# Kernel optimization log

Hardware: AMD Instinct MI355X
Metric: run time of the kernel (lower is better)

The kernel has to match this reference:

```python
import jax, jax.numpy as jnp
import numpy as np

B, N, E, H, AD, V, STEPS = 32, 256, 4, 512, 256, 10000, 5


def setup_inputs() -> dict:
    key = jax.random.key(0)
    ks = jax.random.split(key, 16)
    s = 0.02  # xavier-ish init scale
    return {
        "annotation": jax.random.randint(ks[0], (B, N), 0, V),
        "A": jax.random.normal(ks[1], (B, N, 2 * N * E), dtype=jnp.float32),
        "emb": jax.random.normal(ks[2], (V, AD), dtype=jnp.float32) * s,
        "W_in": jax.random.normal(ks[3], (E, H, H), dtype=jnp.float32) * s,
        "b_in": jnp.zeros((E, H), jnp.float32),
        "W_out": jax.random.normal(ks[4], (E, H, H), dtype=jnp.float32) * s,
        "b_out": jnp.zeros((E, H), jnp.float32),
        "Wr": jax.random.normal(ks[5], (3 * H, H), dtype=jnp.float32) * s,
        "br": jnp.zeros((H,), jnp.float32),
        "Wz": jax.random.normal(ks[6], (3 * H, H), dtype=jnp.float32) * s,
        "bz": jnp.zeros((H,), jnp.float32),
        "Wh": jax.random.normal(ks[7], (3 * H, H), dtype=jnp.float32) * s,
        "bh": jnp.zeros((H,), jnp.float32),
        "Wo": jax.random.normal(ks[8], (H + AD, H), dtype=jnp.float32) * s,
        "bo": jnp.zeros((H,), jnp.float32),
    }


def reference(annotation, A, emb, W_in, b_in, W_out, b_out,
              Wr, br, Wz, bz, Wh, bh, Wo, bo):
    ann = emb[annotation]                                   # [B, N, AD]
    pad = jnp.zeros((B, N, H - AD), ann.dtype)
    prop = jnp.concatenate([ann, pad], axis=2)              # [B, N, H]
    A_in, A_out = A[:, :, :N * E], A[:, :, N * E:]          # [B, N, N*E] each

    for _ in range(STEPS):
        # fused per-edge-type linears: [B, E, N, H] -> [B, E*N, H]
        ins = (jnp.einsum('bnd,edh->benh', prop, W_in)
               + b_in[None, :, None, :]).reshape(B, E * N, H)
        outs = (jnp.einsum('bnd,edh->benh', prop, W_out)
                + b_out[None, :, None, :]).reshape(B, E * N, H)
        a_in = jnp.matmul(A_in, ins)                        # [B, N, H]
        a_out = jnp.matmul(A_out, outs)                     # [B, N, H]
        a = jnp.concatenate([a_in, a_out, prop], axis=2)    # [B, N, 3H]
        r = jax.nn.sigmoid(a @ Wr + br)
        z = jax.nn.sigmoid(a @ Wz + bz)
        j = jnp.concatenate([a_in, a_out, r * prop], axis=2)
        h_hat = jnp.tanh(j @ Wh + bh)
        prop = (1.0 - z) * prop + z * h_hat

    join = jnp.concatenate([prop, ann], axis=2)             # [B, N, H+AD]
    return jnp.tanh(join @ Wo + bo)                         # [B, N, H]
```

## Files before the change

kernel.cpp:

```cpp
#include <hip/hip_runtime.h>
#include <hip/hip_bf16.h>
#include <cstdint>
#include <cstddef>

typedef unsigned short u16;
typedef _Float16 f16;
typedef f16 f16x8 __attribute__((ext_vector_type(8)));
typedef float f32x4 __attribute__((ext_vector_type(4)));

static __device__ inline u16 f2h(float f) {
    f16 h = (f16)f;
    return *reinterpret_cast<u16*>(&h);
}
static __device__ inline float h2f(u16 u) {
    f16 h = *reinterpret_cast<f16*>(&u);
    return (float)h;
}

#define GLL(g, l) __builtin_amdgcn_global_load_lds(                    \
    (const __attribute__((address_space(1))) void*)(g),                \
    (__attribute__((address_space(3))) void*)(l), 16, 0, 0)

static __device__ inline int xcd_swz(int fid, int nwg) {
    const int q = nwg >> 3;
    return (fid & 7) * q + (fid >> 3);
}

static __device__ inline void stage_tile(const u16* __restrict__ src, int ld,
                                         u16* lds, int wave, int lane) {
    const int r = lane >> 2;
    const int c = (lane & 3) << 3;
    const u16* g0 = src + (size_t)(wave * 32 + r) * ld + c;
    GLL(g0, lds + wave * 1024);
    GLL(g0 + (size_t)16 * ld, lds + wave * 1024 + 512);
}

static __device__ inline void compute32(const u16* lA, const u16* lB,
                                        int wq_r, int wq_c, int lr, int lk,
                                        f32x4 acc[4][4]) {
    f16x8 a[4], b[4];
    #pragma unroll
    for (int i = 0; i < 4; ++i)
        a[i] = *reinterpret_cast<const f16x8*>(&lA[(wq_r + i * 16 + lr) * 32 + lk]);
    #pragma unroll
    for (int j = 0; j < 4; ++j)
        b[j] = *reinterpret_cast<const f16x8*>(&lB[(wq_c + j * 16 + lr) * 32 + lk]);
    #pragma unroll
    for (int i = 0; i < 4; ++i)
        #pragma unroll
        for (int j = 0; j < 4; ++j)
            acc[i][j] = __builtin_amdgcn_mfma_f32_16x16x32_f16(a[i], b[j], acc[i][j], 0, 0, 0);
}

static __device__ inline void gemm128(const u16* __restrict__ a1, int lda1, int ka1,
                                      const u16* __restrict__ a2, int lda2,
                                      const u16* __restrict__ bt, int ldb,
                                      int K, int m0, int n0,
                                      u16* sA, u16* sB, f32x4 acc[4][4])
{
    const int t = threadIdx.x, lane = t & 63, wave = t >> 6;
    const int lr = lane & 15, lk = (lane >> 4) << 3;
    const int wq_r = (wave >> 1) << 6, wq_c = (wave & 1) << 6;
    const int nt = K >> 5;
    stage_tile(a1 + (size_t)m0 * lda1, lda1, sA, wave, lane);
    stage_tile(bt + (size_t)n0 * ldb, ldb, sB, wave, lane);
    __syncthreads();
    int buf = 0;
    for (int ti = 0; ti < nt; ++ti) {
        const int k1 = (ti + 1) << 5;
        if (k1 < K) {
            const u16* s;
            int ld;
            if (k1 < ka1) { s = a1 + (size_t)m0 * lda1 + k1;        ld = lda1; }
            else          { s = a2 + (size_t)m0 * lda2 + (k1 - ka1); ld = lda2; }
            stage_tile(s, ld, sA + (buf ^ 1) * 4096, wave, lane);
            stage_tile(bt + (size_t)n0 * ldb + k1, ldb, sB + (buf ^ 1) * 4096, wave, lane);
        }
        compute32(sA + buf * 4096, sB + buf * 4096, wq_r, wq_c, lr, lk, acc);
        __syncthreads();
        buf ^= 1;
    }
}

#define EPI                                         \
    const int lane = threadIdx.x & 63;              \
    const int wave = threadIdx.x >> 6;              \
    const int wq_r = (wave >> 1) << 6;              \
    const int wq_c = (wave & 1) << 6;               \
    const int lr = lane & 15;                       \
    const int l4 = (lane >> 4) << 2;

#define TDIR (32ull * 512 * 1024)

__global__ __launch_bounds__(256, 4) void k_proj(const u16* __restrict__ P,
                                                 const u16* __restrict__ Wio,
                                                 const float* __restrict__ b_in,
                                                 const float* __restrict__ b_out,
                                                 u16* __restrict__ T)
{
    __shared__ u16 sA[2 * 4096], sB[2 * 4096];
    const int fid = xcd_swz(blockIdx.x, gridDim.x);
    const int n = fid & 31, m = fid >> 5;
    const int m0 = m << 7, n0 = n << 7;
    f32x4 acc[4][4] = {};
    gemm128(P, 512, 512, P, 512, Wio, 512, 512, m0, n0, sA, sB, acc);
    EPI
    #pragma unroll
    for (int i = 0; i < 4; ++i) {
        const int row = m0 + wq_r + i * 16 + l4;
        const int b = row >> 8, mm = row & 255;
        #pragma unroll
        for (int j = 0; j < 4; ++j) {
            const int col = n0 + wq_c + j * 16 + lr;
            const int dir = col >> 11, eh = col & 2047;
            const float bia = (dir ? b_out : b_in)[eh];
            const int e = eh >> 9, h = eh & 511;
            ushort4 w4;
            w4.x = f2h(acc[i][j][0] + bia);
            w4.y = f2h(acc[i][j][1] + bia);
            w4.z = f2h(acc[i][j][2] + bia);
            w4.w = f2h(acc[i][j][3] + bia);
            u16* dst = T + (size_t)dir * TDIR + (size_t)b * 512 * 1024 + (size_t)h * 1024 + e * 256 + mm;
            *reinterpret_cast<ushort4*>(dst) = w4;
        }
    }
}

__global__ __launch_bounds__(256, 4) void k_amat(const u16* __restrict__ A16,
                                                 const u16* __restrict__ T,
                                                 u16* __restrict__ acat)
{
    __shared__ u16 sA[2 * 4096], sB[2 * 4096];
    const int fid = xcd_swz(blockIdx.x, gridDim.x);
    const int n = fid & 3, m = (fid >> 2) & 1, bd = fid >> 3;
    const int b = bd >> 1, dir = bd & 1;
    const int m0 = m << 7, n0 = n << 7;
    const u16* A1 = A16 + (size_t)b * 256 * 2048 + dir * 1024;
    const u16* Bt = T + (size_t)dir * TDIR + (size_t)b * 512 * 1024;
    f32x4 acc[4][4] = {};
    gemm128(A1, 2048, 1024, A1, 2048, Bt, 1024, 1024, m0, n0, sA, sB, acc);
    EPI
    #pragma unroll
    for (int i = 0; i < 4; ++i) {
        const int row = m0 + wq_r + i * 16 + l4;
        #pragma unroll
        for (int j = 0; j < 4; ++j) {
            const int col = n0 + wq_c + j * 16 + lr;
            #pragma unroll
            for (int v = 0; v < 4; ++v)
                acat[((size_t)b * 256 + row + v) * 1024 + dir * 512 + col] = f2h(acc[i][j][v]);
        }
    }
}

__global__ __launch_bounds__(256, 4) void k_gates(const u16* __restrict__ acat,
                                                  const u16* __restrict__ P,
                                                  const u16* __restrict__ Wrzh,
                                                  const float* __restrict__ br,
                                                  const float* __restrict__ bz,
                                                  u16* __restrict__ rp,
                                                  float* __restrict__ z,
                                                  float* __restrict__ hpart)
{
    __shared__ u16 sA[2 * 4096], sB[2 * 4096];
    const int fid = xcd_swz(blockIdx.x, gridDim.x);
    const int n = fid % 12, m = fid / 12;
    const int m0 = m << 7, n0 = n << 7;
    f32x4 acc[4][4] = {};
    gemm128(acat, 1024, 1024, P, 512, Wrzh, 1536, 1536, m0, n0, sA, sB, acc);
    EPI
    #pragma unroll
    for (int i = 0; i < 4; ++i) {
        const int row = m0 + wq_r + i * 16 + l4;
        #pragma unroll
        for (int j = 0; j < 4; ++j) {
            const int col = n0 + wq_c + j * 16 + lr;
            if (col < 512) {
                const float bia = br[col];
                #pragma unroll
                for (int v = 0; v < 4; ++v) {
                    const float s = 1.0f / (1.0f + __expf(-(acc[i][j][v] + bia)));
                    const size_t idx = (size_t)(row + v) * 512 + col;
                    rp[idx] = f2h(s * h2f(P[idx]));
                }
            } else if (col < 1024) {
                const float bia = bz[col - 512];
                #pragma unroll
                for (int v = 0; v < 4; ++v)
                    z[(size_t)(row + v) * 512 + (col - 512)] =
                        1.0f / (1.0f + __expf(-(acc[i][j][v] + bia)));
            } else {
                #pragma unroll
                for (int v = 0; v < 4; ++v)
                    hpart[(size_t)(row + v) * 512 + (col - 1024)] = acc[i][j][v];
            }
        }
    }
}

__global__ __launch_bounds__(256, 4) void k_hup(const u16* __restrict__ rp,
                                                const u16* __restrict__ WhP,
                                                const float* __restrict__ bh,
                                                const float* __restrict__ z,
                                                const float* __restrict__ hpart,
                                                u16* __restrict__ P)
{
    __shared__ u16 sA[2 * 4096], sB[2 * 4096];
    const int fid = xcd_swz(blockIdx.x, gridDim.x);
    const int n = fid & 3, m = fid >> 2;
    const int m0 = m << 7, n0 = n << 7;
    f32x4 acc[4][4] = {};
    gemm128(rp, 512, 512, rp, 512, WhP, 512, 512, m0, n0, sA, sB, acc);
    EPI
    #pragma unroll
    for (int i = 0; i < 4; ++i) {
        const int row = m0 + wq_r + i * 16 + l4;
        #pragma unroll
        for (int j = 0; j < 4; ++j) {
            const int col = n0 + wq_c + j * 16 + lr;
            const float bia = bh[col];
            #pragma unroll
            for (int v = 0; v < 4; ++v) {
                const size_t idx = (size_t)(row + v) * 512 + col;
                const float hh = tanhf(hpart[idx] + acc[i][j][v] + bia);
                const float zz = z[idx];
                const float pn = (1.0f - zz) * h2f(P[idx]) + zz * hh;
                P[idx] = f2h(pn);
            }
        }
    }
}

__global__ __launch_bounds__(256, 4) void k_final(const u16* __restrict__ P,
                                                  const u16* __restrict__ annf,
                                                  const u16* __restrict__ Wj,
                                                  const float* __restrict__ bo,
                                                  float* __restrict__ out)
{
    __shared__ u16 sA[2 * 4096], sB[2 * 4096];
    const int fid = xcd_swz(blockIdx.x, gridDim.x);
    const int n = fid & 3, m = fid >> 2;
    const int m0 = m << 7, n0 = n << 7;
    f32x4 acc[4][4] = {};
    gemm128(P, 512, 512, annf, 256, Wj, 768, 768, m0, n0, sA, sB, acc);
    EPI
    #pragma unroll
    for (int i = 0; i < 4; ++i) {
        const int row = m0 + wq_r + i * 16 + l4;
        #pragma unroll
        for (int j = 0; j < 4; ++j) {
            const int col = n0 + wq_c + j * 16 + lr;
            const float bia = bo[col];
            #pragma unroll
            for (int v = 0; v < 4; ++v)
                out[(size_t)(row + v) * 512 + col] = tanhf(acc[i][j][v] + bia);
        }
    }
}

__global__ void s_gather(const int* __restrict__ ann, const float* __restrict__ emb,
                         u16* __restrict__ P, u16* __restrict__ annf)
{
    const int gid = blockIdx.x * 256 + threadIdx.x;
    const int row = gid >> 9, d = gid & 511;
    float v = 0.0f;
    if (d < 256) v = emb[(size_t)ann[row] * 256 + d];
    const u16 h = f2h(v);
    P[gid] = h;
    if (d < 256) annf[((size_t)row << 8) + d] = h;
}

__global__ void s_cvtA(const float* __restrict__ src, u16* __restrict__ dst)
{
    const size_t base = ((size_t)blockIdx.x * 256 + threadIdx.x) * 8;
    float4 f0 = *reinterpret_cast<const float4*>(src + base);
    float4 f1 = *reinterpret_cast<const float4*>(src + base + 4);
    ushort4 p0 = { f2h(f0.x), f2h(f0.y), f2h(f0.z), f2h(f0.w) };
    ushort4 p1 = { f2h(f1.x), f2h(f1.y), f2h(f1.z), f2h(f1.w) };
    *reinterpret_cast<ushort4*>(dst + base)     = p0;
    *reinterpret_cast<ushort4*>(dst + base + 4) = p1;
}

__global__ void s_wio(const float* __restrict__ Wi, const float* __restrict__ Wo,
                      u16* __restrict__ dst)
{
    const int gid = blockIdx.x * 256 + threadIdx.x;
    if (gid >= 4096 * 512) return;
    const int nn = gid >> 9, k = gid & 511;
    const int dir = nn >> 11, e = (nn >> 9) & 3, h = nn & 511;
    const float* W = dir ? Wo : Wi;
    dst[gid] = f2h(W[(size_t)e * 512 * 512 + (size_t)k * 512 + h]);
}

__global__ void s_wrzh(const float* __restrict__ Wr, const float* __restrict__ Wz,
                       const float* __restrict__ Wh, u16* __restrict__ dst)
{
    const int gid = blockIdx.x * 256 + threadIdx.x;
    if (gid >= 1536 * 1536) return;
    const int nn = gid / 1536, k = gid - nn * 1536;
    float v;
    if (nn < 512)       v = Wr[(size_t)k * 512 + nn];
    else if (nn < 1024) v = Wz[(size_t)k * 512 + (nn - 512)];
    else                v = (k < 1024) ? Wh[(size_t)k * 512 + (nn - 1024)] : 0.0f;
    dst[gid] = f2h(v);
}

__global__ void s_whp(const float* __restrict__ Wh, u16* __restrict__ dst)
{
    const int gid = blockIdx.x * 256 + threadIdx.x;
    if (gid >= 512 * 512) return;
    const int nn = gid >> 9, k = gid & 511;
    dst[gid] = f2h(Wh[(size_t)(1024 + k) * 512 + nn]);
}

__global__ void s_wj(const float* __restrict__ Wo, u16* __restrict__ dst)
{
    const int gid = blockIdx.x * 256 + threadIdx.x;
    if (gid >= 512 * 768) return;
    const int nn = gid / 768, k = gid - nn * 768;
    dst[gid] = f2h(Wo[(size_t)k * 512 + nn]);
}

extern "C" void kernel_launch(void* const* d_in, const int* in_sizes, int n_in,
                              void* d_out, int out_size, void* d_ws, size_t ws_size,
                              hipStream_t stream) {
    const int*   ann   = (const int*)d_in[0];
    const float* A     = (const float*)d_in[1];
    const float* emb   = (const float*)d_in[2];
    const float* W_in  = (const float*)d_in[3];
    const float* b_in  = (const float*)d_in[4];
    const float* W_out = (const float*)d_in[5];
    const float* b_out = (const float*)d_in[6];
    const float* Wr    = (const float*)d_in[7];
    const float* br    = (const float*)d_in[8];
    const float* Wz    = (const float*)d_in[9];
    const float* bz    = (const float*)d_in[10];
    const float* Wh    = (const float*)d_in[11];
    const float* bh    = (const float*)d_in[12];
    const float* Wo    = (const float*)d_in[13];
    const float* bo    = (const float*)d_in[14];
    float* out = (float*)d_out;

    char* ws = (char*)d_ws;
    size_t off = 0;
    auto alloc = [&](size_t bytes) -> void* {
        void* p = ws + off;
        off = (off + bytes + 255) & ~(size_t)255;
        return p;
    };
    float* z_f32 = (float*)alloc(8192ull * 512 * 4);
    float* hpart = (float*)alloc(8192ull * 512 * 4);
    u16* P     = (u16*)alloc(8192ull * 512 * 2);
    u16* rp    = (u16*)alloc(8192ull * 512 * 2);
    u16* annf  = (u16*)alloc(8192ull * 256 * 2);
    u16* acat  = (u16*)alloc(8192ull * 1024 * 2);
    u16* A16   = (u16*)alloc(8192ull * 2048 * 2);
    u16* T     = (u16*)alloc(2 * TDIR * 2);
    u16* WioT  = (u16*)alloc(4096ull * 512 * 2);
    u16* WrzhT = (u16*)alloc(1536ull * 1536 * 2);
    u16* WhPT  = (u16*)alloc(512ull * 512 * 2);
    u16* WjT   = (u16*)alloc(512ull * 768 * 2);

    s_gather<<<16384, 256, 0, stream>>>(ann, emb, P, annf);
    s_cvtA<<<8192, 256, 0, stream>>>(A, A16);
    s_wio<<<(4096 * 512 + 255) / 256, 256, 0, stream>>>(W_in, W_out, WioT);
    s_wrzh<<<(1536 * 1536 + 255) / 256, 256, 0, stream>>>(Wr, Wz, Wh, WrzhT);
    s_whp<<<(512 * 512 + 255) / 256, 256, 0, stream>>>(Wh, WhPT);
    s_wj<<<(512 * 768 + 255) / 256, 256, 0, stream>>>(Wo, WjT);

    for (int s = 0; s < 5; ++s) {
        k_proj<<<2048, 256, 0, stream>>>(P, WioT, b_in, b_out, T);
        k_amat<<<512, 256, 0, stream>>>(A16, T, acat);
        k_gates<<<768, 256, 0, stream>>>(acat, P, WrzhT, br, bz, rp, z_f32, hpart);
        k_hup<<<256, 256, 0, stream>>>(rp, WhPT, bh, z_f32, hpart, P);
    }
    k_final<<<256, 256, 0, stream>>>(P, annf, WjT, bo, out);
}
```

Baseline: 965.4 us.

## Swizzle LDS tiles, skip zero K blocks, store gate intermediates in fp16

Applies an XOR swizzle to the LDS tile layout in both the global-to-LDS staging and the fragment reads, to reduce bank conflicts. Cuts K to 256 for the first projection step, where the upper half of P is zero padding. In the h-columns of the gate GEMM it skips the last K third, which multiplies the zero-weight prop block. It also stores z and the h partial in fp16 instead of fp32 to halve that traffic, at some precision cost.

```diff
diff --git a/kernel.cpp b/kernel.cpp
--- a/kernel.cpp
+++ b/kernel.cpp
@@ -8,11 +8,11 @@
 typedef f16 f16x8 __attribute__((ext_vector_type(8)));
 typedef float f32x4 __attribute__((ext_vector_type(4)));
 
-static __device__ inline u16 f2h(float f) {
+static __device__ __forceinline__ u16 f2h(float f) {
     f16 h = (f16)f;
     return *reinterpret_cast<u16*>(&h);
 }
-static __device__ inline float h2f(u16 u) {
+static __device__ __forceinline__ float h2f(u16 u) {
     f16 h = *reinterpret_cast<f16*>(&u);
     return (float)h;
 }
@@ -21,30 +21,33 @@
     (const __attribute__((address_space(1))) void*)(g),                \
     (__attribute__((address_space(3))) void*)(l), 16, 0, 0)
 
-static __device__ inline int xcd_swz(int fid, int nwg) {
+static __device__ __forceinline__ int xcd_swz(int fid, int nwg) {
     const int q = nwg >> 3;
     return (fid & 7) * q + (fid >> 3);
 }
 
-static __device__ inline void stage_tile(const u16* __restrict__ src, int ld,
-                                         u16* lds, int wave, int lane) {
+#define TDIR (32ull * 512 * 1024)
+
+static __device__ __forceinline__ void stage_tile(const u16* __restrict__ src, int ld,
+                                                  u16* lds, int wave, int lane) {
     const int r = lane >> 2;
-    const int c = (lane & 3) << 3;
+    const int c = ((lane & 3) << 3) ^ ((r & 3) << 3);
     const u16* g0 = src + (size_t)(wave * 32 + r) * ld + c;
     GLL(g0, lds + wave * 1024);
     GLL(g0 + (size_t)16 * ld, lds + wave * 1024 + 512);
 }
 
-static __device__ inline void compute32(const u16* lA, const u16* lB,
-                                        int wq_r, int wq_c, int lr, int lk,
-                                        f32x4 acc[4][4]) {
+static __device__ __forceinline__ void compute32(const u16* lA, const u16* lB,
+                                                 int wq_r, int wq_c, int lr, int lk,
+                                                 f32x4 acc[4][4]) {
+    const int ce = lk ^ ((lr & 3) << 3);
     f16x8 a[4], b[4];
     #pragma unroll
     for (int i = 0; i < 4; ++i)
-        a[i] = *reinterpret_cast<const f16x8*>(&lA[(wq_r + i * 16 + lr) * 32 + lk]);
+        a[i] = *reinterpret_cast<const f16x8*>(&lA[(wq_r + i * 16 + lr) * 32 + ce]);
     #pragma unroll
     for (int j = 0; j < 4; ++j)
-        b[j] = *reinterpret_cast<const f16x8*>(&lB[(wq_c + j * 16 + lr) * 32 + lk]);
+        b[j] = *reinterpret_cast<const f16x8*>(&lB[(wq_c + j * 16 + lr) * 32 + ce]);
     #pragma unroll
     for (int i = 0; i < 4; ++i)
         #pragma unroll
@@ -52,11 +55,11 @@
             acc[i][j] = __builtin_amdgcn_mfma_f32_16x16x32_f16(a[i], b[j], acc[i][j], 0, 0, 0);
 }
 
-static __device__ inline void gemm128(const u16* __restrict__ a1, int lda1, int ka1,
-                                      const u16* __restrict__ a2, int lda2,
-                                      const u16* __restrict__ bt, int ldb,
-                                      int K, int m0, int n0,
-                                      u16* sA, u16* sB, f32x4 acc[4][4])
+static __device__ __forceinline__ void gemm128(const u16* __restrict__ a1, int lda1, int ka1,
+                                               const u16* __restrict__ a2, int lda2,
+                                               const u16* __restrict__ bt, int ldb,
+                                               int K, int m0, int n0,
+                                               u16* sA, u16* sB, f32x4 acc[4][4])
 {
     const int t = threadIdx.x, lane = t & 63, wave = t >> 6;
     const int lr = lane & 15, lk = (lane >> 4) << 3;
@@ -71,7 +74,7 @@
         if (k1 < K) {
             const u16* s;
             int ld;
-            if (k1 < ka1) { s = a1 + (size_t)m0 * lda1 + k1;        ld = lda1; }
+            if (k1 < ka1) { s = a1 + (size_t)m0 * lda1 + k1;         ld = lda1; }
             else          { s = a2 + (size_t)m0 * lda2 + (k1 - ka1); ld = lda2; }
             stage_tile(s, ld, sA + (buf ^ 1) * 4096, wave, lane);
             stage_tile(bt + (size_t)n0 * ldb + k1, ldb, sB + (buf ^ 1) * 4096, wave, lane);
@@ -90,20 +93,18 @@
     const int lr = lane & 15;                       \
     const int l4 = (lane >> 4) << 2;
 
-#define TDIR (32ull * 512 * 1024)
-
 __global__ __launch_bounds__(256, 4) void k_proj(const u16* __restrict__ P,
                                                  const u16* __restrict__ Wio,
                                                  const float* __restrict__ b_in,
                                                  const float* __restrict__ b_out,
-                                                 u16* __restrict__ T)
+                                                 u16* __restrict__ T, int K)
 {
     __shared__ u16 sA[2 * 4096], sB[2 * 4096];
     const int fid = xcd_swz(blockIdx.x, gridDim.x);
     const int n = fid & 31, m = fid >> 5;
     const int m0 = m << 7, n0 = n << 7;
     f32x4 acc[4][4] = {};
-    gemm128(P, 512, 512, P, 512, Wio, 512, 512, m0, n0, sA, sB, acc);
+    gemm128(P, 512, 512, P, 512, Wio, 512, K, m0, n0, sA, sB, acc);
     EPI
     #pragma unroll
     for (int i = 0; i < 4; ++i) {
@@ -114,14 +115,14 @@
             const int col = n0 + wq_c + j * 16 + lr;
             const int dir = col >> 11, eh = col & 2047;
             const float bia = (dir ? b_out : b_in)[eh];
-            const int e = eh >> 9, h = eh & 511;
+            const int e = eh >> 9, hh = eh & 511;
             ushort4 w4;
             w4.x = f2h(acc[i][j][0] + bia);
             w4.y = f2h(acc[i][j][1] + bia);
             w4.z = f2h(acc[i][j][2] + bia);
             w4.w = f2h(acc[i][j][3] + bia);
-            u16* dst = T + (size_t)dir * TDIR + (size_t)b * 512 * 1024 + (size_t)h * 1024 + e * 256 + mm;
-            *reinterpret_cast<ushort4*>(dst) = w4;
+            *reinterpret_cast<ushort4*>(&T[(size_t)dir * TDIR + (size_t)b * 512 * 1024
+                                           + (size_t)hh * 1024 + e * 256 + mm]) = w4;
         }
     }
 }
@@ -159,15 +160,16 @@
                                                   const float* __restrict__ br,
                                                   const float* __restrict__ bz,
                                                   u16* __restrict__ rp,
-                                                  float* __restrict__ z,
-                                                  float* __restrict__ hpart)
+                                                  u16* __restrict__ z16,
+                                                  u16* __restrict__ hp16)
 {
     __shared__ u16 sA[2 * 4096], sB[2 * 4096];
     const int fid = xcd_swz(blockIdx.x, gridDim.x);
     const int n = fid % 12, m = fid / 12;
     const int m0 = m << 7, n0 = n << 7;
-    f32x4 acc[4][4] = {};
-    gemm128(acat, 1024, 1024, P, 512, Wrzh, 1536, 1536, m0, n0, sA, sB, acc);
+    const int K = (n0 >= 1024) ? 1024 : 1536;
+    f32x4 acc[4][4] = {};
+    gemm128(acat, 1024, 1024, P, 512, Wrzh, 1536, K, m0, n0, sA, sB, acc);
     EPI
     #pragma unroll
     for (int i = 0; i < 4; ++i) {
@@ -187,12 +189,12 @@
                 const float bia = bz[col - 512];
                 #pragma unroll
                 for (int v = 0; v < 4; ++v)
-                    z[(size_t)(row + v) * 512 + (col - 512)] =
-                        1.0f / (1.0f + __expf(-(acc[i][j][v] + bia)));
+                    z16[(size_t)(row + v) * 512 + (col - 512)] =
+                        f2h(1.0f / (1.0f + __expf(-(acc[i][j][v] + bia))));
             } else {
                 #pragma unroll
                 for (int v = 0; v < 4; ++v)
-                    hpart[(size_t)(row + v) * 512 + (col - 1024)] = acc[i][j][v];
+                    hp16[(size_t)(row + v) * 512 + (col - 1024)] = f2h(acc[i][j][v]);
             }
         }
     }
@@ -201,8 +203,8 @@
 __global__ __launch_bounds__(256, 4) void k_hup(const u16* __restrict__ rp,
                                                 const u16* __restrict__ WhP,
                                                 const float* __restrict__ bh,
-                                                const float* __restrict__ z,
-                                                const float* __restrict__ hpart,
+                                                const u16* __restrict__ z16,
+                                                const u16* __restrict__ hp16,
                                                 u16* __restrict__ P)
 {
     __shared__ u16 sA[2 * 4096], sB[2 * 4096];
@@ -222,8 +224,8 @@
             #pragma unroll
             for (int v = 0; v < 4; ++v) {
                 const size_t idx = (size_t)(row + v) * 512 + col;
-                const float hh = tanhf(hpart[idx] + acc[i][j][v] + bia);
-                const float zz = z[idx];
+                const float hh = tanhf(h2f(hp16[idx]) + acc[i][j][v] + bia);
+                const float zz = h2f(z16[idx]);
                 const float pn = (1.0f - zz) * h2f(P[idx]) + zz * hh;
                 P[idx] = f2h(pn);
             }
@@ -348,8 +350,8 @@
         off = (off + bytes + 255) & ~(size_t)255;
         return p;
     };
-    float* z_f32 = (float*)alloc(8192ull * 512 * 4);
-    float* hpart = (float*)alloc(8192ull * 512 * 4);
+    u16* z16   = (u16*)alloc(8192ull * 512 * 2);
+    u16* hp16  = (u16*)alloc(8192ull * 512 * 2);
     u16* P     = (u16*)alloc(8192ull * 512 * 2);
     u16* rp    = (u16*)alloc(8192ull * 512 * 2);
     u16* annf  = (u16*)alloc(8192ull * 256 * 2);
@@ -369,10 +371,10 @@
     s_wj<<<(512 * 768 + 255) / 256, 256, 0, stream>>>(Wo, WjT);
 
     for (int s = 0; s < 5; ++s) {
-        k_proj<<<2048, 256, 0, stream>>>(P, WioT, b_in, b_out, T);
+        k_proj<<<2048, 256, 0, stream>>>(P, WioT, b_in, b_out, T, s == 0 ? 256 : 512);
         k_amat<<<512, 256, 0, stream>>>(A16, T, acat);
-        k_gates<<<768, 256, 0, stream>>>(acat, P, WrzhT, br, bz, rp, z_f32, hpart);
-        k_hup<<<256, 256, 0, stream>>>(rp, WhPT, bh, z_f32, hpart, P);
+        k_gates<<<768, 256, 0, stream>>>(acat, P, WrzhT, br, bz, rp, z16, hp16);
+        k_hup<<<256, 256, 0, stream>>>(rp, WhPT, bh, z16, hp16, P);
     }
     k_final<<<256, 256, 0, stream>>>(P, annf, WjT, bo, out);
 }
```

Measured after the change: 914.7 us. -5.3%, faster.
